# Kernel tuning notes

Measured on AMD Instinct MI355X. Metric: run time of the kernel, lower is better.

Reference implementation:

```python
import jax, jax.numpy as jnp
import numpy as np

B, T, C, H = 8, 4096, 384, 64

def setup_inputs() -> dict:
    key = jax.random.key(0)
    k1, k2, k3, k4 = jax.random.split(key, 4)
    x = jax.random.normal(k1, (B, T, C), dtype=jnp.float32)
    # nn.Linear(C, H, bias=False) weight applied as x @ W (W stored [C, H])
    s = 1.0 / np.sqrt(C)
    Wk = jax.random.normal(k2, (C, H), dtype=jnp.float32) * s
    Wq = jax.random.normal(k3, (C, H), dtype=jnp.float32) * s
    Wv = jax.random.normal(k4, (C, H), dtype=jnp.float32) * s
    return {"x": x, "Wk": Wk, "Wq": Wq, "Wv": Wv}

def reference(x, Wk, Wq, Wv):
    Bx, Tx, Cx = x.shape
    k = x @ Wk  # [B,T,H]
    q = x @ Wq  # [B,T,H]
    v = x @ Wv  # [B,T,H]
    # NOTE: original scales by C**-0.5 (embedding dim), not head_size**-0.5
    w = jnp.einsum('bth,bsh->bts', q, k) * (Cx ** -0.5)  # [B,T,T]
    causal = jnp.tril(jnp.ones((Tx, Tx), dtype=bool))
    w = jnp.where(causal, w, -jnp.inf)
    w = jax.nn.softmax(w, axis=-1)
    # dropout omitted (eval mode / deterministic reference)
    out = jnp.einsum('bts,bsh->bth', w, v)  # [B,T,H]
    return out
```

## Files before the change

kernel.cpp:

```cpp
#include <hip/hip_runtime.h>
#include <hip/hip_bf16.h>


typedef __bf16 bf16x8 __attribute__((ext_vector_type(8)));
typedef float  f32x4  __attribute__((ext_vector_type(4)));

#define BB   8
#define TT   4096
#define CC   384
#define HH   64
#define NROW (BB*TT)
#define QSCALE (0.05103103630798288f * 1.4426950408889634f)

#if __has_builtin(__builtin_amdgcn_exp2f)
#define EXP2(x) __builtin_amdgcn_exp2f(x)
#else
#define EXP2(x) exp2f(x)
#endif

#define LDS_ROUNDTRIP_FENCE() __asm volatile("s_waitcnt lgkmcnt(0)" ::: "memory")

__device__ __forceinline__ unsigned short f2bf(float f) {
    __bf16 h = (__bf16)f;
    return __builtin_bit_cast(unsigned short, h);
}

__global__ __launch_bounds__(256) void wtrans_kernel(
        const float* __restrict__ Wk,
        const float* __restrict__ Wq,
        const float* __restrict__ Wv,
        unsigned short* __restrict__ Wt) {
    __shared__ __align__(16) unsigned short tile[64][72];
    const float* Wm = (blockIdx.y == 0) ? Wk : ((blockIdx.y == 1) ? Wq : Wv);
    unsigned short* Wtm = Wt + blockIdx.y * (HH * CC);
    const int c0 = blockIdx.x * 64;
#pragma unroll
    for (int i = 0; i < 16; ++i) {
        int id = threadIdx.x + i * 256;
        int c = id >> 6, h = id & 63;
        tile[c][h] = f2bf(Wm[(c0 + c) * HH + h]);
    }
    __syncthreads();
#pragma unroll
    for (int i = 0; i < 16; ++i) {
        int id = threadIdx.x + i * 256;
        int h = id >> 6, c = id & 63;
        Wtm[h * CC + c0 + c] = tile[c][h];
    }
}

__global__ __launch_bounds__(512, 4) void qkv_kernel(
        const float* __restrict__ x,
        const unsigned short* __restrict__ Wt,
        unsigned short* __restrict__ q_ws,
        unsigned short* __restrict__ k_ws,
        unsigned short* __restrict__ vt_ws) {
    __shared__ __align__(16) f32x4 xacc[256 * 13];
    __shared__ __align__(16) unsigned short vtile[64][72];

    const int lane = threadIdx.x & 63;
    const int wv8  = threadIdx.x >> 6;
    const int grp  = wv8 >> 2;
    const int wg   = wv8 & 3;
    const int g256 = threadIdx.x & 255;
    const int l15  = lane & 15;
    const int quad = lane >> 4;
    const int rb   = blockIdx.x * 64;
    const int row  = rb + wg * 16 + l15;

    const float* xbase = x + (long)row * CC + grp * 192 + quad * 8;
    float4 xr[12];
#pragma unroll
    for (int i = 0; i < 6; ++i) {
        xr[2 * i]     = *reinterpret_cast<const float4*>(xbase + i * 32);
        xr[2 * i + 1] = *reinterpret_cast<const float4*>(xbase + i * 32 + 4);
    }
    bf16x8 a[6];
#pragma unroll
    for (int i = 0; i < 6; ++i) {
        a[i][0] = (__bf16)xr[2 * i].x;     a[i][1] = (__bf16)xr[2 * i].y;
        a[i][2] = (__bf16)xr[2 * i].z;     a[i][3] = (__bf16)xr[2 * i].w;
        a[i][4] = (__bf16)xr[2 * i + 1].x; a[i][5] = (__bf16)xr[2 * i + 1].y;
        a[i][6] = (__bf16)xr[2 * i + 1].z; a[i][7] = (__bf16)xr[2 * i + 1].w;
    }

    f32x4 acc[3][4];
    const f32x4 zero = {0.f, 0.f, 0.f, 0.f};
#pragma unroll
    for (int m = 0; m < 3; ++m)
#pragma unroll
        for (int nt = 0; nt < 4; ++nt) acc[m][nt] = zero;

#pragma unroll
    for (int i = 0; i < 6; ++i) {
        const int gcoff = grp * 192 + i * 32 + quad * 8;
#pragma unroll
        for (int m = 0; m < 3; ++m) {
            const unsigned short* wtm = Wt + m * (HH * CC);
#pragma unroll
            for (int nt = 0; nt < 4; ++nt) {
                bf16x8 bfr = *reinterpret_cast<const bf16x8*>(
                    wtm + (nt * 16 + l15) * CC + gcoff);
                acc[m][nt] = __builtin_amdgcn_mfma_f32_16x16x32_bf16(
                    a[i], bfr, acc[m][nt], 0, 0, 0);
            }
        }
    }

    const int cidx = g256 * 13;
    if (grp == 1) {
#pragma unroll
        for (int m = 0; m < 3; ++m)
#pragma unroll
            for (int nt = 0; nt < 4; ++nt)
                xacc[cidx + m * 4 + nt] = acc[m][nt];
    }
    __syncthreads();

    if (grp == 0) {
#pragma unroll
        for (int m = 0; m < 3; ++m)
#pragma unroll
            for (int nt = 0; nt < 4; ++nt)
                acc[m][nt] += xacc[cidx + m * 4 + nt];

        const int rt = (rb >> 4) + wg;
#pragma unroll
        for (int nt = 0; nt < 4; ++nt) {
            const int h  = nt * 16 + l15;
            const int c8 = h >> 3;
            const int jj = h & 7;
#pragma unroll
            for (int r = 0; r < 4; ++r) {
                const int gr = rb + wg * 16 + quad * 4 + r;
                const int ii = quad * 4 + r;
                k_ws[((rt * 8 + c8) * 16 + ii) * 8 + jj] = f2bf(acc[0][nt][r]);
                q_ws[gr * HH + h] = f2bf(acc[1][nt][r] * QSCALE);
                vtile[h][ii + wg * 16] = f2bf(acc[2][nt][r]);
            }
        }
    }
    __syncthreads();
    {
        int id = threadIdx.x;
        int dt = id >> 7, sc = (id >> 4) & 7, ii = id & 15;
        unsigned short* dst = vt_ws + (long)(rb >> 6) * 4096
                              + (dt * 8 + sc) * 128 + ii * 8;
        *reinterpret_cast<uint4*>(dst) =
            *reinterpret_cast<const uint4*>(&vtile[dt * 16 + ii][sc * 8]);
    }
}

__global__ __launch_bounds__(1024, 4) void attn_kernel(
        const unsigned short* __restrict__ q_ws,
        const unsigned short* __restrict__ k_ws,
        const unsigned short* __restrict__ vt_ws,
        float* __restrict__ out) {
    __shared__ __align__(16) unsigned short P_lds[16 * 16 * 64];
    __shared__ __align__(16) float xchg[64 * 65];
    __shared__ float mx1[64], lx1[64];

    const int lane = threadIdx.x & 63;
    const int wv16 = threadIdx.x >> 6;
    const int grp  = wv16 >> 2;
    const int wg   = wv16 & 3;
    const int l15  = lane & 15;
    const int quad = lane >> 4;

    const int bid = blockIdx.x;
    const int b   = bid & 7;
    const int p   = bid >> 3;

    const f32x4 zero = {0.f, 0.f, 0.f, 0.f};
    const int pbase = wv16 * 1024 + l15 * 64;
    const int pxor  = (l15 & 7) << 3;

    auto do_tile = [&](int t, int qt, int qrow,
                       const bf16x8& qf0, const bf16x8& qf1,
                       f32x4* o, float& mprev, float& lsum) {
        const int s0 = t * 64;
        const unsigned short* ktile = k_ws + ((long)((b * TT + s0) >> 4)) * 1024;
        const unsigned short* vtile = vt_ws + ((long)((b * TT + s0) >> 6)) * 4096;

        bf16x8 ka0[4], ka1[4];
#pragma unroll
        for (int st = 0; st < 4; ++st) {
            ka0[st] = *reinterpret_cast<const bf16x8*>(
                ktile + ((st * 8 + quad) * 16 + l15) * 8);
            ka1[st] = *reinterpret_cast<const bf16x8*>(
                ktile + ((st * 8 + 4 + quad) * 16 + l15) * 8);
        }
        bf16x8 vb0[4], vb1[4];
#pragma unroll
        for (int dt = 0; dt < 4; ++dt) {
            vb0[dt] = *reinterpret_cast<const bf16x8*>(
                vtile + dt * 1024 + quad * 128 + l15 * 8);
            vb1[dt] = *reinterpret_cast<const bf16x8*>(
                vtile + dt * 1024 + (4 + quad) * 128 + l15 * 8);
        }

        f32x4 sc[4];
#pragma unroll
        for (int st = 0; st < 4; ++st) {
            f32x4 z = zero;
            z = __builtin_amdgcn_mfma_f32_16x16x32_bf16(ka0[st], qf0, z, 0, 0, 0);
            z = __builtin_amdgcn_mfma_f32_16x16x32_bf16(ka1[st], qf1, z, 0, 0, 0);
            sc[st] = z;
        }

        if (t == qt) {
#pragma unroll
            for (int st = 0; st < 4; ++st)
#pragma unroll
                for (int r = 0; r < 4; ++r) {
                    int sg = s0 + st * 16 + quad * 4 + r;
                    if (sg > qrow) sc[st][r] = -1e30f;
                }
        }

        float mloc = -1e30f;
#pragma unroll
        for (int st = 0; st < 4; ++st)
#pragma unroll
            for (int r = 0; r < 4; ++r) mloc = fmaxf(mloc, sc[st][r]);
        mloc = fmaxf(mloc, __shfl_xor(mloc, 16));
        mloc = fmaxf(mloc, __shfl_xor(mloc, 32));
        const float mnew = fmaxf(mprev, mloc);
        const unsigned long long anych = __ballot(mnew > mprev);
        float alpha = 1.0f;
        if (anych) alpha = EXP2(mprev - mnew);

        float psum = 0.f;
#pragma unroll
        for (int st = 0; st < 4; ++st) {
            union { unsigned short us[4]; uint2 u2; } pk;
#pragma unroll
            for (int r = 0; r < 4; ++r) {
                float pv = EXP2(sc[st][r] - mnew);
                psum += pv;
                pk.us[r] = f2bf(pv);
            }
            *reinterpret_cast<uint2*>(
                &P_lds[pbase + ((st * 16 + quad * 4) ^ pxor)]) = pk.u2;
        }
        psum += __shfl_xor(psum, 16);
        psum += __shfl_xor(psum, 32);
        lsum = lsum * alpha + psum;
        mprev = mnew;

        if (anych) {
            float ar[4];
#pragma unroll
            for (int r = 0; r < 4; ++r) ar[r] = __shfl(alpha, quad * 4 + r);
#pragma unroll
            for (int dt = 0; dt < 4; ++dt)
#pragma unroll
                for (int r = 0; r < 4; ++r) o[dt][r] *= ar[r];
        }

        LDS_ROUNDTRIP_FENCE();

        bf16x8 pf0 = *reinterpret_cast<const bf16x8*>(
            &P_lds[pbase + ((quad * 8) ^ pxor)]);
        bf16x8 pf1 = *reinterpret_cast<const bf16x8*>(
            &P_lds[pbase + ((32 + quad * 8) ^ pxor)]);
#pragma unroll
        for (int dt = 0; dt < 4; ++dt) {
            o[dt] = __builtin_amdgcn_mfma_f32_16x16x32_bf16(pf0, vb0[dt], o[dt], 0, 0, 0);
            o[dt] = __builtin_amdgcn_mfma_f32_16x16x32_bf16(pf1, vb1[dt], o[dt], 0, 0, 0);
        }
    };

    auto merge_store = [&](int qt, f32x4* o, float& mprev, float& lsum) {
        for (int rr = 1; rr < 4; ++rr) {
            __syncthreads();
            if (grp == rr) {
                if (quad == 0) { mx1[wg * 16 + l15] = mprev; lx1[wg * 16 + l15] = lsum; }
#pragma unroll
                for (int dt = 0; dt < 4; ++dt)
#pragma unroll
                    for (int r = 0; r < 4; ++r)
                        xchg[(wg * 16 + quad * 4 + r) * 65 + dt * 16 + l15] = o[dt][r];
            }
            __syncthreads();
            if (grp == 0) {
#pragma unroll
                for (int r = 0; r < 4; ++r) {
                    const int row = wg * 16 + quad * 4 + r;
                    const float m0r = __shfl(mprev, quad * 4 + r);
                    const float m1r = mx1[row];
                    const float ms  = fmaxf(m0r, m1r);
                    const float w0  = EXP2(m0r - ms);
                    const float w1  = EXP2(m1r - ms);
#pragma unroll
                    for (int dt = 0; dt < 4; ++dt)
                        o[dt][r] = o[dt][r] * w0 + xchg[row * 65 + dt * 16 + l15] * w1;
                }
                const float m1l = mx1[wg * 16 + l15];
                const float msl = fmaxf(mprev, m1l);
                lsum = EXP2(mprev - msl) * lsum + EXP2(m1l - msl) * lx1[wg * 16 + l15];
                mprev = msl;
            }
        }
        if (grp == 0) {
            float rl[4];
#pragma unroll
            for (int r = 0; r < 4; ++r) rl[r] = 1.0f / __shfl(lsum, quad * 4 + r);
            const int orow = qt * 64 + wg * 16 + quad * 4;
#pragma unroll
            for (int dt = 0; dt < 4; ++dt)
#pragma unroll
                for (int r = 0; r < 4; ++r)
                    out[(long)(b * TT + orow + r) * HH + dt * 16 + l15] = o[dt][r] * rl[r];
        }
        __syncthreads();
    };

    {
        const int qt = 63 - p;
        const int qrow = qt * 64 + wg * 16 + l15;
        const unsigned short* qbase = q_ws + (b * TT + qrow) * HH;
        const bf16x8 qf0 = *reinterpret_cast<const bf16x8*>(qbase + quad * 8);
        const bf16x8 qf1 = *reinterpret_cast<const bf16x8*>(qbase + 32 + quad * 8);
        f32x4 o[4];
#pragma unroll
        for (int dt = 0; dt < 4; ++dt) o[dt] = zero;
        float mprev = -1e30f, lsum = 0.f;
        for (int t = grp; t <= qt; t += 4)
            do_tile(t, qt, qrow, qf0, qf1, o, mprev, lsum);
        merge_store(qt, o, mprev, lsum);
    }

    {
        const int qt = p;
        const int qrow = qt * 64 + wg * 16 + l15;
        const unsigned short* qbase = q_ws + (b * TT + qrow) * HH;
        const bf16x8 qf0 = *reinterpret_cast<const bf16x8*>(qbase + quad * 8);
        const bf16x8 qf1 = *reinterpret_cast<const bf16x8*>(qbase + 32 + quad * 8);
        f32x4 o[4];
#pragma unroll
        for (int dt = 0; dt < 4; ++dt) o[dt] = zero;
        float mprev = -1e30f, lsum = 0.f;
        for (int t = grp; t <= qt; t += 4)
            do_tile(t, qt, qrow, qf0, qf1, o, mprev, lsum);
        merge_store(qt, o, mprev, lsum);
    }
}

extern "C" void kernel_launch(void* const* d_in, const int* in_sizes, int n_in,
                              void* d_out, int out_size, void* d_ws, size_t ws_size,
                              hipStream_t stream) {
    const float* x  = (const float*)d_in[0];
    const float* Wk = (const float*)d_in[1];
    const float* Wq = (const float*)d_in[2];
    const float* Wv = (const float*)d_in[3];
    float* out = (float*)d_out;

    char* ws = (char*)d_ws;
    unsigned short* Wt    = (unsigned short*)(ws);
    unsigned short* q_ws  = (unsigned short*)(ws + 147456);
    unsigned short* k_ws  = (unsigned short*)(ws + 147456 + 4194304);
    unsigned short* vt_ws = (unsigned short*)(ws + 147456 + 2 * 4194304);

    wtrans_kernel<<<dim3(6, 3), 256, 0, stream>>>(Wk, Wq, Wv, Wt);
    qkv_kernel<<<NROW / 64, 512, 0, stream>>>(x, Wt, q_ws, k_ws, vt_ws);
    attn_kernel<<<(TT / 128) * BB, 1024, 0, stream>>>(q_ws, k_ws, vt_ws, out);
}
```

Baseline: 165.3 us.

## Permute K key layout so softmax probabilities feed PV MFMA from registers

```diff
diff --git a/kernel.cpp b/kernel.cpp
--- a/kernel.cpp
+++ b/kernel.cpp
@@ -17,8 +17,6 @@
 #else
 #define EXP2(x) exp2f(x)
 #endif
-
-#define LDS_ROUNDTRIP_FENCE() __asm volatile("s_waitcnt lgkmcnt(0)" ::: "memory")
 
 __device__ __forceinline__ unsigned short f2bf(float f) {
     __bf16 h = (__bf16)f;
@@ -124,7 +122,6 @@
             for (int nt = 0; nt < 4; ++nt)
                 acc[m][nt] += xacc[cidx + m * 4 + nt];
 
-        const int rt = (rb >> 4) + wg;
 #pragma unroll
         for (int nt = 0; nt < 4; ++nt) {
             const int h  = nt * 16 + l15;
@@ -134,7 +131,11 @@
             for (int r = 0; r < 4; ++r) {
                 const int gr = rb + wg * 16 + quad * 4 + r;
                 const int ii = quad * 4 + r;
-                k_ws[((rt * 8 + c8) * 16 + ii) * 8 + jj] = f2bf(acc[0][nt][r]);
+                const int s   = gr & 63;
+                const int stp = ((s >> 4) & 2) + ((s >> 2) & 1);
+                const int ip  = ((s >> 1) & 12) + (s & 3);
+                k_ws[(long)(gr >> 6) * 4096 + stp * 1024 + c8 * 128 + ip * 8 + jj]
+                    = f2bf(acc[0][nt][r]);
                 q_ws[gr * HH + h] = f2bf(acc[1][nt][r] * QSCALE);
                 vtile[h][ii + wg * 16] = f2bf(acc[2][nt][r]);
             }
@@ -156,7 +157,6 @@
         const unsigned short* __restrict__ k_ws,
         const unsigned short* __restrict__ vt_ws,
         float* __restrict__ out) {
-    __shared__ __align__(16) unsigned short P_lds[16 * 16 * 64];
     __shared__ __align__(16) float xchg[64 * 65];
     __shared__ float mx1[64], lx1[64];
 
@@ -172,8 +172,6 @@
     const int p   = bid >> 3;
 
     const f32x4 zero = {0.f, 0.f, 0.f, 0.f};
-    const int pbase = wv16 * 1024 + l15 * 64;
-    const int pxor  = (l15 & 7) << 3;
 
     auto do_tile = [&](int t, int qt, int qrow,
                        const bf16x8& qf0, const bf16x8& qf1,
@@ -213,7 +211,8 @@
             for (int st = 0; st < 4; ++st)
 #pragma unroll
                 for (int r = 0; r < 4; ++r) {
-                    int sg = s0 + st * 16 + quad * 4 + r;
+                    int sg = s0 + ((st >> 1) << 5) + (quad << 3)
+                               + ((st & 1) << 2) + r;
                     if (sg > qrow) sc[st][r] = -1e30f;
                 }
         }
@@ -232,17 +231,13 @@
 
         float psum = 0.f;
 #pragma unroll
-        for (int st = 0; st < 4; ++st) {
-            union { unsigned short us[4]; uint2 u2; } pk;
+        for (int st = 0; st < 4; ++st)
 #pragma unroll
             for (int r = 0; r < 4; ++r) {
                 float pv = EXP2(sc[st][r] - mnew);
                 psum += pv;
-                pk.us[r] = f2bf(pv);
-            }
-            *reinterpret_cast<uint2*>(
-                &P_lds[pbase + ((st * 16 + quad * 4) ^ pxor)]) = pk.u2;
-        }
+                sc[st][r] = pv;
+            }
         psum += __shfl_xor(psum, 16);
         psum += __shfl_xor(psum, 32);
         lsum = lsum * alpha + psum;
@@ -258,12 +253,14 @@
                 for (int r = 0; r < 4; ++r) o[dt][r] *= ar[r];
         }
 
-        LDS_ROUNDTRIP_FENCE();
-
-        bf16x8 pf0 = *reinterpret_cast<const bf16x8*>(
-            &P_lds[pbase + ((quad * 8) ^ pxor)]);
-        bf16x8 pf1 = *reinterpret_cast<const bf16x8*>(
-            &P_lds[pbase + ((32 + quad * 8) ^ pxor)]);
+        bf16x8 pf0, pf1;
+#pragma unroll
+        for (int r = 0; r < 4; ++r) {
+            pf0[r]     = (__bf16)sc[0][r];
+            pf0[4 + r] = (__bf16)sc[1][r];
+            pf1[r]     = (__bf16)sc[2][r];
+            pf1[4 + r] = (__bf16)sc[3][r];
+        }
 #pragma unroll
         for (int dt = 0; dt < 4; ++dt) {
             o[dt] = __builtin_amdgcn_mfma_f32_16x16x32_bf16(pf0, vb0[dt], o[dt], 0, 0, 0);
```

After: 164.1 us. Within noise of the previous version (-0.7%).
